# Optimization experiments

Hardware: AMD Instinct MI355X
Metric: run time of the kernel (lower is better)

The kernel has to match this reference:

```python
import jax, jax.numpy as jnp
import numpy as np

N_EMBD = 1024
N_HEAD = 16
HEAD_SIZE = N_EMBD // N_HEAD  # 64
HEAD_INDEX = 0
# ALiBi slope: x = (2**8)**(1/n_head); slope = 1 / x**(head_index+1)
SLOPE = 1.0 / ((2.0 ** 8) ** (1.0 / N_HEAD)) ** (HEAD_INDEX + 1)
B, T = 4, 4096


def setup_inputs() -> dict:
    key = jax.random.key(0)
    kx, kq, kk, kv = jax.random.split(key, 4)
    x = jax.random.normal(kx, (B, T, N_EMBD), dtype=jnp.float32)
    wq = jax.random.normal(kq, (HEAD_SIZE, N_EMBD), dtype=jnp.float32) * 0.02
    wk = jax.random.normal(kk, (HEAD_SIZE, N_EMBD), dtype=jnp.float32) * 0.02
    wv = jax.random.normal(kv, (HEAD_SIZE, N_EMBD), dtype=jnp.float32) * 0.02
    return {"x": x, "wq": wq, "wk": wk, "wv": wv}


def reference(x, wq, wk, wv):
    Bq, Tq, C = x.shape
    q = jnp.einsum('btc,hc->bth', x, wq)  # [B,T,Hd]
    k = jnp.einsum('btc,hc->bth', x, wk)
    v = jnp.einsum('btc,hc->bth', x, wv)
    # NOTE: original scales by C**-0.5 where C = n_embd (full dim), not head_size
    wei = jnp.einsum('bth,bsh->bts', q, k) * (C ** -0.5)  # [B,T,T]
    idx = jnp.arange(Tq)
    distance = idx[None, :] - idx[:, None]  # [T,T], j - i
    wei = wei + distance.astype(wei.dtype) * jnp.asarray(SLOPE, wei.dtype)
    causal = distance <= 0  # tril: key index j <= query index i
    wei = jnp.where(causal[None, :, :], wei, -jnp.inf)
    wei = jax.nn.softmax(wei, axis=-1)
    out = jnp.einsum('bts,bsh->bth', wei, v)  # [B,T,Hd]
    return out
```

## Files before the change

kernel.cpp:

```cpp
#include <hip/hip_runtime.h>
#include <hip/hip_bf16.h>
#include <stdint.h>
#include <math.h>

typedef __attribute__((ext_vector_type(8))) short bf16x8;
typedef __attribute__((ext_vector_type(4))) float f32x4;

#define TSEQ 4096
#define LOG2E 1.44269504088896340736f
#define SLOPE 0.70710678118654752440f
#define SL2E (SLOPE * LOG2E)

__device__ __forceinline__ unsigned short f32_to_bf16(float f) {
  union { float f; unsigned int u; } v; v.f = f;
  unsigned int r = v.u + 0x7fffu + ((v.u >> 16) & 1u);
  return (unsigned short)(r >> 16);
}

__device__ __forceinline__ unsigned int pk2(float a, float b) {
  union { __hip_bfloat162 h; unsigned int u; } c;
  c.h = __float22bfloat162_rn(make_float2(a, b));
  return c.u;
}
__device__ __forceinline__ bf16x8 cvt8(f32x4 a, f32x4 b) {
  union { unsigned int u[4]; bf16x8 v; } r;
  r.u[0] = pk2(a[0], a[1]); r.u[1] = pk2(a[2], a[3]);
  r.u[2] = pk2(b[0], b[1]); r.u[3] = pk2(b[2], b[3]);
  return r.v;
}

__device__ __forceinline__ void async_cp16(const void* g, void* l) {
  __builtin_amdgcn_global_load_lds(
      (const __attribute__((address_space(1))) unsigned int*)g,
      (__attribute__((address_space(3))) unsigned int*)l, 16, 0, 0);
}

__global__ __launch_bounds__(256) void init_kernel(
    const float* __restrict__ wq, const float* __restrict__ wk,
    const float* __restrict__ wv, unsigned short* __restrict__ Wb) {
  int tid = blockIdx.x * 256 + threadIdx.x;
  if (tid >= 24576) return;
  int lane = tid & 63, s = (tid >> 6) & 31, nt = (tid >> 11) & 3, t = tid >> 13;
  int n = nt * 16 + (lane & 15);
  int k = s * 32 + (lane >> 4) * 8;
  const float* src = (t == 0 ? wq : (t == 1 ? wk : wv)) + (size_t)n * 1024 + k;
  f32x4 a = *(const f32x4*)src;
  f32x4 b = *(const f32x4*)(src + 4);
  if (t == 0) {
#pragma unroll
    for (int j = 0; j < 4; ++j) { a[j] *= 0.03125f; b[j] *= 0.03125f; }
  }
  *(bf16x8*)(Wb + (size_t)tid * 8) = cvt8(a, b);
}

__global__ __launch_bounds__(512, 2) void proj_kernel(
    const float* __restrict__ x, const unsigned short* __restrict__ Wb,
    unsigned short* __restrict__ qb, unsigned short* __restrict__ kb,
    unsigned short* __restrict__ vt) {
  __shared__ float xb[8][2][16][64];

  const int tix = threadIdx.x;
  const int lane = tix & 63;
  const int wave = tix >> 6;
  const int wr = wave >> 1;
  const int wc = wave & 1;
  const int l16 = lane & 15, quad = lane >> 4;
  const int R0 = blockIdx.x * 64;

  f32x4 acc[6];
#pragma unroll
  for (int i = 0; i < 6; ++i) acc[i] = (f32x4){0.f, 0.f, 0.f, 0.f};

  const float* xsrc[4];
#pragma unroll
  for (int c = 0; c < 4; ++c) {
    int rg = c * 4 + quad;
    int g = l16 ^ (rg & 15);
    xsrc[c] = x + (size_t)(R0 + wr * 16 + rg) * 1024 + g * 4;
  }
  const unsigned short* wsrc[6];
#pragma unroll
  for (int cc = 0; cc < 6; ++cc)
    wsrc[cc] = Wb + ((size_t)((wc * 6 + cc) * 32) * 64 + lane) * 8;

  auto stage = [&](int s, int bi) {
#pragma unroll
    for (int c = 0; c < 4; ++c)
      async_cp16(xsrc[c] + s * 64, &xb[wave][bi][c * 4][0]);
  };

  stage(0, 0);

#pragma unroll 2
  for (int s = 0; s < 16; ++s) {
    const int cur = s & 1;
    bf16x8 w[6][2];
#pragma unroll
    for (int cc = 0; cc < 6; ++cc)
#pragma unroll
      for (int ss = 0; ss < 2; ++ss)
        w[cc][ss] = *(const bf16x8*)(wsrc[cc] + (size_t)(2 * s + ss) * 512);
    __builtin_amdgcn_sched_barrier(0);
    if (s + 1 < 16) stage(s + 1, 1 - cur);
    __builtin_amdgcn_sched_barrier(0);
    if (s + 1 < 16) asm volatile("s_waitcnt vmcnt(4)" ::: "memory");
    else            asm volatile("s_waitcnt vmcnt(0)" ::: "memory");
    __builtin_amdgcn_sched_barrier(0);
#pragma unroll
    for (int ss = 0; ss < 2; ++ss) {
      const float* base = &xb[wave][cur][l16][0];
      f32x4 a0 = *(const f32x4*)(base + ((ss * 8 + quad * 2) ^ l16) * 4);
      f32x4 a1 = *(const f32x4*)(base + ((ss * 8 + quad * 2 + 1) ^ l16) * 4);
      bf16x8 af = cvt8(a0, a1);
#pragma unroll
      for (int cc = 0; cc < 6; ++cc)
        acc[cc] = __builtin_amdgcn_mfma_f32_16x16x32_bf16(
            af, w[cc][ss], acc[cc], 0, 0, 0);
    }
    __builtin_amdgcn_sched_barrier(0);
  }

#pragma unroll
  for (int cc = 0; cc < 6; ++cc) {
    const int ci = wc * 6 + cc;
#pragma unroll
    for (int r = 0; r < 4; ++r) {
      int row = R0 + wr * 16 + quad * 4 + r;
      unsigned short hv = f32_to_bf16(acc[cc][r]);
      if (ci < 4) {
        qb[(size_t)row * 64 + ci * 16 + l16] = hv;
      } else if (ci < 8) {
        kb[(size_t)row * 64 + (ci - 4) * 16 + l16] = hv;
      } else {
        int b = row >> 12, tt = row & 4095;
        vt[((size_t)b * 64 + (ci - 8) * 16 + l16) * TSEQ + tt] = hv;
      }
    }
  }
}

__global__ __launch_bounds__(64) void attn_kernel(
    const unsigned short* __restrict__ qb, const unsigned short* __restrict__ kb,
    const unsigned short* __restrict__ vt, float* __restrict__ out) {
  __shared__ unsigned short pbuf[16][40];

  const int lane = threadIdx.x & 63;
  const int l16 = lane & 15, quad = lane >> 4;
  const int tid = blockIdx.x;
  const int b = tid & 3;
  const int r0 = (tid >> 2) << 4;
  const int j0 = (r0 >= 16) ? (r0 - 16) : 0;

  const unsigned short* kbase = kb + (size_t)b * TSEQ * 64;
  const unsigned short* vbase = vt + (size_t)b * 64 * TSEQ;

  const unsigned short* qrow = qb + (size_t)(b * TSEQ + r0 + l16) * 64 + quad * 8;
  bf16x8 qa0 = *(const bf16x8*)qrow;
  bf16x8 qa1 = *(const bf16x8*)(qrow + 32);

  f32x4 o[5];
#pragma unroll
  for (int dt = 0; dt < 5; ++dt) o[dt] = (f32x4){0.f, 0.f, 0.f, 0.f};

  const int irel = j0 + l16 - r0 - quad * 4;
  const float fb = SL2E * (float)irel;

#pragma unroll
  for (int nt = 0; nt < 2; ++nt) {
    const unsigned short* krow = kbase + (size_t)(j0 + nt * 16 + l16) * 64 + quad * 8;
    f32x4 sa = (f32x4){0.f, 0.f, 0.f, 0.f};
    sa = __builtin_amdgcn_mfma_f32_16x16x32_bf16(qa0, *(const bf16x8*)krow, sa, 0, 0, 0);
    sa = __builtin_amdgcn_mfma_f32_16x16x32_bf16(qa1, *(const bf16x8*)(krow + 32), sa, 0, 0, 0);
#pragma unroll
    for (int r = 0; r < 4; ++r) {
      float arg = fmaf(sa[r], LOG2E, fb + SL2E * (float)(nt * 16 - r));
      float p = exp2f(arg);
      if (irel + nt * 16 - r > 0) p = 0.f;
      pbuf[quad * 4 + r][nt * 16 + l16] = f32_to_bf16(p);
    }
  }
  bf16x8 pa = *(const bf16x8*)&pbuf[l16][quad * 8];

#pragma unroll
  for (int dt = 0; dt < 4; ++dt) {
    const unsigned short* vrow = vbase + (size_t)(dt * 16 + l16) * TSEQ + j0 + quad * 8;
    o[dt] = __builtin_amdgcn_mfma_f32_16x16x32_bf16(pa, *(const bf16x8*)vrow, o[dt], 0, 0, 0);
  }
  {
    union { unsigned int u[4]; bf16x8 v; } ones;
    ones.u[0] = ones.u[1] = ones.u[2] = ones.u[3] = 0x3F803F80u;
    o[4] = __builtin_amdgcn_mfma_f32_16x16x32_bf16(pa, ones.v, o[4], 0, 0, 0);
  }

#pragma unroll
  for (int r = 0; r < 4; ++r) {
    const float invl = 1.0f / o[4][r];
    const int row = b * TSEQ + r0 + quad * 4 + r;
#pragma unroll
    for (int dt = 0; dt < 4; ++dt)
      out[(size_t)row * 64 + dt * 16 + l16] = o[dt][r] * invl;
  }
}

extern "C" void kernel_launch(void* const* d_in, const int* in_sizes, int n_in,
                              void* d_out, int out_size, void* d_ws, size_t ws_size,
                              hipStream_t stream) {
  const float* x  = (const float*)d_in[0];
  const float* wq = (const float*)d_in[1];
  const float* wk = (const float*)d_in[2];
  const float* wv = (const float*)d_in[3];
  float* out = (float*)d_out;

  char* ws = (char*)d_ws;
  unsigned short* Wb = (unsigned short*)(ws);
  unsigned short* qb = (unsigned short*)(ws + 393216);
  unsigned short* kb = (unsigned short*)(ws + 393216 + 2097152);
  unsigned short* vt = (unsigned short*)(ws + 393216 + 2 * 2097152);

  init_kernel<<<96, 256, 0, stream>>>(wq, wk, wv, Wb);
  proj_kernel<<<256, 512, 0, stream>>>(x, Wb, qb, kb, vt);
  attn_kernel<<<1024, 64, 0, stream>>>(qb, kb, vt, out);
}
```

Baseline: 128.2 us.

## Load x directly into registers with register double-buffering in projection

Removes the LDS staging of x via global_load_lds in the projection kernel. Each lane now loads its own x fragment straight from global memory into registers, and x and W loads are double-buffered in registers across steps. This drops the LDS round trip, the explicit waitcnt and the sched barriers, and relaxes the launch bound's occupancy hint. In exchange register pressure rises, and the per-lane global loads are strided across rows, which may coalesce less well than the previous swizzled LDS path.

Result: slower. 133.8 us (+4.4%).

```diff
diff --git a/kernel.cpp b/kernel.cpp
--- a/kernel.cpp
+++ b/kernel.cpp
@@ -27,12 +27,6 @@
   r.u[0] = pk2(a[0], a[1]); r.u[1] = pk2(a[2], a[3]);
   r.u[2] = pk2(b[0], b[1]); r.u[3] = pk2(b[2], b[3]);
   return r.v;
-}
-
-__device__ __forceinline__ void async_cp16(const void* g, void* l) {
-  __builtin_amdgcn_global_load_lds(
-      (const __attribute__((address_space(1))) unsigned int*)g,
-      (__attribute__((address_space(3))) unsigned int*)l, 16, 0, 0);
 }
 
 __global__ __launch_bounds__(256) void init_kernel(
@@ -53,12 +47,10 @@
   *(bf16x8*)(Wb + (size_t)tid * 8) = cvt8(a, b);
 }
 
-__global__ __launch_bounds__(512, 2) void proj_kernel(
+__global__ __launch_bounds__(512) void proj_kernel(
     const float* __restrict__ x, const unsigned short* __restrict__ Wb,
     unsigned short* __restrict__ qb, unsigned short* __restrict__ kb,
     unsigned short* __restrict__ vt) {
-  __shared__ float xb[8][2][16][64];
-
   const int tix = threadIdx.x;
   const int lane = tix & 63;
   const int wave = tix >> 6;
@@ -71,53 +63,48 @@
 #pragma unroll
   for (int i = 0; i < 6; ++i) acc[i] = (f32x4){0.f, 0.f, 0.f, 0.f};
 
-  const float* xsrc[4];
-#pragma unroll
-  for (int c = 0; c < 4; ++c) {
-    int rg = c * 4 + quad;
-    int g = l16 ^ (rg & 15);
-    xsrc[c] = x + (size_t)(R0 + wr * 16 + rg) * 1024 + g * 4;
-  }
+  const float* xrow = x + (size_t)(R0 + wr * 16 + l16) * 1024 + quad * 8;
   const unsigned short* wsrc[6];
 #pragma unroll
   for (int cc = 0; cc < 6; ++cc)
     wsrc[cc] = Wb + ((size_t)((wc * 6 + cc) * 32) * 64 + lane) * 8;
 
-  auto stage = [&](int s, int bi) {
-#pragma unroll
-    for (int c = 0; c < 4; ++c)
-      async_cp16(xsrc[c] + s * 64, &xb[wave][bi][c * 4][0]);
+  struct XS { f32x4 a[2][2]; };
+  auto load_x = [&](int s, XS& xo) {
+#pragma unroll
+    for (int ss = 0; ss < 2; ++ss) {
+      xo.a[ss][0] = *(const f32x4*)(xrow + s * 64 + ss * 32);
+      xo.a[ss][1] = *(const f32x4*)(xrow + s * 64 + ss * 32 + 4);
+    }
   };
-
-  stage(0, 0);
-
-#pragma unroll 2
-  for (int s = 0; s < 16; ++s) {
-    const int cur = s & 1;
-    bf16x8 w[6][2];
+  auto load_w = [&](int s, bf16x8 (&w)[6][2]) {
 #pragma unroll
     for (int cc = 0; cc < 6; ++cc)
 #pragma unroll
       for (int ss = 0; ss < 2; ++ss)
         w[cc][ss] = *(const bf16x8*)(wsrc[cc] + (size_t)(2 * s + ss) * 512);
-    __builtin_amdgcn_sched_barrier(0);
-    if (s + 1 < 16) stage(s + 1, 1 - cur);
-    __builtin_amdgcn_sched_barrier(0);
-    if (s + 1 < 16) asm volatile("s_waitcnt vmcnt(4)" ::: "memory");
-    else            asm volatile("s_waitcnt vmcnt(0)" ::: "memory");
-    __builtin_amdgcn_sched_barrier(0);
+  };
+  auto compute = [&](XS& xi, bf16x8 (&w)[6][2]) {
 #pragma unroll
     for (int ss = 0; ss < 2; ++ss) {
-      const float* base = &xb[wave][cur][l16][0];
-      f32x4 a0 = *(const f32x4*)(base + ((ss * 8 + quad * 2) ^ l16) * 4);
-      f32x4 a1 = *(const f32x4*)(base + ((ss * 8 + quad * 2 + 1) ^ l16) * 4);
-      bf16x8 af = cvt8(a0, a1);
+      bf16x8 af = cvt8(xi.a[ss][0], xi.a[ss][1]);
 #pragma unroll
       for (int cc = 0; cc < 6; ++cc)
         acc[cc] = __builtin_amdgcn_mfma_f32_16x16x32_bf16(
             af, w[cc][ss], acc[cc], 0, 0, 0);
     }
-    __builtin_amdgcn_sched_barrier(0);
+  };
+
+  XS xA, xB;
+  bf16x8 wA[6][2], wB[6][2];
+  load_x(0, xA);
+  load_w(0, wA);
+#pragma unroll 1
+  for (int sp = 0; sp < 16; sp += 2) {
+    if (sp + 1 < 16) { load_x(sp + 1, xB); load_w(sp + 1, wB); }
+    compute(xA, wA);
+    if (sp + 2 < 16) { load_x(sp + 2, xA); load_w(sp + 2, wA); }
+    compute(xB, wB);
   }
 
 #pragma unroll
```

## Restructure projection kernel into smaller blocks with async LDS staging of weights

Applied to the files above, without the earlier changes.

The projection kernel now runs 1024 blocks of 256 threads, each covering 16 rows instead of 64. Each wave computes 3 of the 12 output column tiles rather than 6. Weight fragments are no longer loaded straight into registers: they are copied asynchronously into LDS alongside the x tiles, double-buffered two stages ahead. The aim is better CU occupancy and deeper latency hiding for the global loads. The cost is that each wave stages the same x rows separately, which raises redundant x traffic through L2, and the extra LDS buffers may limit occupancy.

Measured after the change: 129.2 us. Within noise of the previous version (+0.8%).

```diff
diff --git a/kernel.cpp b/kernel.cpp
--- a/kernel.cpp
+++ b/kernel.cpp
@@ -53,80 +53,87 @@
   *(bf16x8*)(Wb + (size_t)tid * 8) = cvt8(a, b);
 }
 
-__global__ __launch_bounds__(512, 2) void proj_kernel(
+__global__ __launch_bounds__(256, 2) void proj_kernel(
     const float* __restrict__ x, const unsigned short* __restrict__ Wb,
     unsigned short* __restrict__ qb, unsigned short* __restrict__ kb,
     unsigned short* __restrict__ vt) {
-  __shared__ float xb[8][2][16][64];
+  __shared__ float xlds[4][2][16][64];
+  __shared__ unsigned short wlds[4][2][6][64][8];
 
   const int tix = threadIdx.x;
   const int lane = tix & 63;
-  const int wave = tix >> 6;
-  const int wr = wave >> 1;
-  const int wc = wave & 1;
+  const int wc = tix >> 6;
   const int l16 = lane & 15, quad = lane >> 4;
-  const int R0 = blockIdx.x * 64;
-
-  f32x4 acc[6];
-#pragma unroll
-  for (int i = 0; i < 6; ++i) acc[i] = (f32x4){0.f, 0.f, 0.f, 0.f};
+  const int R0 = blockIdx.x * 16;
+
+  f32x4 acc0 = {0.f, 0.f, 0.f, 0.f};
+  f32x4 acc1 = {0.f, 0.f, 0.f, 0.f};
+  f32x4 acc2 = {0.f, 0.f, 0.f, 0.f};
 
   const float* xsrc[4];
 #pragma unroll
   for (int c = 0; c < 4; ++c) {
     int rg = c * 4 + quad;
     int g = l16 ^ (rg & 15);
-    xsrc[c] = x + (size_t)(R0 + wr * 16 + rg) * 1024 + g * 4;
-  }
-  const unsigned short* wsrc[6];
-#pragma unroll
-  for (int cc = 0; cc < 6; ++cc)
-    wsrc[cc] = Wb + ((size_t)((wc * 6 + cc) * 32) * 64 + lane) * 8;
-
-  auto stage = [&](int s, int bi) {
+    xsrc[c] = x + (size_t)(R0 + rg) * 1024 + g * 4;
+  }
+  const unsigned short* wsrc[3];
+#pragma unroll
+  for (int cc = 0; cc < 3; ++cc)
+    wsrc[cc] = Wb + ((size_t)((wc * 3 + cc) * 32) * 64 + lane) * 8;
+
+  auto issue = [&](int s, int bi) {
 #pragma unroll
     for (int c = 0; c < 4; ++c)
-      async_cp16(xsrc[c] + s * 64, &xb[wave][bi][c * 4][0]);
+      async_cp16(xsrc[c] + s * 64, &xlds[wc][bi][c * 4][0]);
+#pragma unroll
+    for (int cc = 0; cc < 3; ++cc)
+#pragma unroll
+      for (int ss = 0; ss < 2; ++ss)
+        async_cp16(wsrc[cc] + (size_t)(2 * s + ss) * 512,
+                   &wlds[wc][bi][cc * 2 + ss][0][0]);
   };
-
-  stage(0, 0);
-
-#pragma unroll 2
-  for (int s = 0; s < 16; ++s) {
-    const int cur = s & 1;
-    bf16x8 w[6][2];
-#pragma unroll
-    for (int cc = 0; cc < 6; ++cc)
-#pragma unroll
-      for (int ss = 0; ss < 2; ++ss)
-        w[cc][ss] = *(const bf16x8*)(wsrc[cc] + (size_t)(2 * s + ss) * 512);
-    __builtin_amdgcn_sched_barrier(0);
-    if (s + 1 < 16) stage(s + 1, 1 - cur);
-    __builtin_amdgcn_sched_barrier(0);
-    if (s + 1 < 16) asm volatile("s_waitcnt vmcnt(4)" ::: "memory");
-    else            asm volatile("s_waitcnt vmcnt(0)" ::: "memory");
-    __builtin_amdgcn_sched_barrier(0);
+  auto compute = [&](int bi) {
+    const float* base = &xlds[wc][bi][l16][0];
 #pragma unroll
     for (int ss = 0; ss < 2; ++ss) {
-      const float* base = &xb[wave][cur][l16][0];
       f32x4 a0 = *(const f32x4*)(base + ((ss * 8 + quad * 2) ^ l16) * 4);
       f32x4 a1 = *(const f32x4*)(base + ((ss * 8 + quad * 2 + 1) ^ l16) * 4);
       bf16x8 af = cvt8(a0, a1);
-#pragma unroll
-      for (int cc = 0; cc < 6; ++cc)
-        acc[cc] = __builtin_amdgcn_mfma_f32_16x16x32_bf16(
-            af, w[cc][ss], acc[cc], 0, 0, 0);
-    }
+      acc0 = __builtin_amdgcn_mfma_f32_16x16x32_bf16(
+          af, *(const bf16x8*)&wlds[wc][bi][0 + ss][lane][0], acc0, 0, 0, 0);
+      acc1 = __builtin_amdgcn_mfma_f32_16x16x32_bf16(
+          af, *(const bf16x8*)&wlds[wc][bi][2 + ss][lane][0], acc1, 0, 0, 0);
+      acc2 = __builtin_amdgcn_mfma_f32_16x16x32_bf16(
+          af, *(const bf16x8*)&wlds[wc][bi][4 + ss][lane][0], acc2, 0, 0, 0);
+    }
+  };
+
+  issue(0, 0);
+  issue(1, 1);
+#pragma unroll 1
+  for (int s = 0; s < 16; ++s) {
+    if (s < 15) asm volatile("s_waitcnt vmcnt(10)" ::: "memory");
+    else        asm volatile("s_waitcnt vmcnt(0)" ::: "memory");
     __builtin_amdgcn_sched_barrier(0);
-  }
-
-#pragma unroll
-  for (int cc = 0; cc < 6; ++cc) {
-    const int ci = wc * 6 + cc;
+    compute(s & 1);
+    __builtin_amdgcn_sched_barrier(0);
+    if (s + 2 < 16) {
+      asm volatile("s_waitcnt lgkmcnt(0)" ::: "memory");
+      __builtin_amdgcn_sched_barrier(0);
+      issue(s + 2, s & 1);
+    }
+    __builtin_amdgcn_sched_barrier(0);
+  }
+
+#pragma unroll
+  for (int cc = 0; cc < 3; ++cc) {
+    const int ci = wc * 3 + cc;
+    const f32x4 a = (cc == 0) ? acc0 : (cc == 1) ? acc1 : acc2;
 #pragma unroll
     for (int r = 0; r < 4; ++r) {
-      int row = R0 + wr * 16 + quad * 4 + r;
-      unsigned short hv = f32_to_bf16(acc[cc][r]);
+      int row = R0 + quad * 4 + r;
+      unsigned short hv = f32_to_bf16(a[r]);
       if (ci < 4) {
         qb[(size_t)row * 64 + ci * 16 + l16] = hv;
       } else if (ci < 8) {
@@ -218,6 +225,6 @@
   unsigned short* vt = (unsigned short*)(ws + 393216 + 2 * 2097152);
 
   init_kernel<<<96, 256, 0, stream>>>(wq, wk, wv, Wb);
-  proj_kernel<<<256, 512, 0, stream>>>(x, Wb, qb, kb, vt);
+  proj_kernel<<<1024, 256, 0, stream>>>(x, Wb, qb, kb, vt);
   attn_kernel<<<1024, 64, 0, stream>>>(qb, kb, vt, out);
 }
```
